# Optimization experiments

Measured on AMD Instinct MI355X. Metric: run time of the kernel, lower is better.

## Reference

```python
import jax, jax.numpy as jnp
import numpy as np

B, L, IDIM = 2, 4096, 2048
N_HEADS, N_GROUPS, HEAD_DIM = 16, 4, 128
GROUP_SIZE = N_HEADS // N_GROUPS
WINDOW = 1024
SCALE = 256.0 ** -0.5  # query_pre_attn_scalar = 256
EPS = 1e-6


def setup_inputs() -> dict:
    key = jax.random.key(0)
    ks = jax.random.split(key, 8)
    x = jax.random.normal(ks[0], (B, L, IDIM), dtype=jnp.float32)
    # realistic RoPE tables
    inv_freq = 1.0 / (10000.0 ** (np.arange(0, HEAD_DIM, 2, dtype=np.float32) / HEAD_DIM))
    t = np.arange(L, dtype=np.float32)
    freqs = np.outer(t, inv_freq)                      # [L, HEAD_DIM//2]
    emb = np.concatenate([freqs, freqs], axis=-1)      # [L, HEAD_DIM]
    cos = jnp.asarray(np.cos(emb), dtype=jnp.float32)
    sin = jnp.asarray(np.sin(emb), dtype=jnp.float32)
    s = 0.02
    Wq = jax.random.normal(ks[1], (IDIM, N_HEADS * HEAD_DIM), dtype=jnp.float32) * s
    Wk = jax.random.normal(ks[2], (IDIM, N_GROUPS * HEAD_DIM), dtype=jnp.float32) * s
    Wv = jax.random.normal(ks[3], (IDIM, N_GROUPS * HEAD_DIM), dtype=jnp.float32) * s
    Wo = jax.random.normal(ks[4], (N_HEADS * HEAD_DIM, IDIM), dtype=jnp.float32) * s
    qn_w = jnp.ones((HEAD_DIM,), dtype=jnp.float32)
    kn_w = jnp.ones((HEAD_DIM,), dtype=jnp.float32)
    return {"x": x, "cos": cos, "sin": sin, "Wq": Wq, "Wk": Wk, "Wv": Wv, "Wo": Wo, "qn_w": qn_w, "kn_w": kn_w}


def _rmsnorm(x, w):
    var = jnp.mean(jnp.square(x), axis=-1, keepdims=True)
    return x * jax.lax.rsqrt(var + EPS) * w


def _rope(x, cos, sin):
    # x: [b, h, l, d]; cos/sin: [l, d]
    d2 = x.shape[-1] // 2
    x1, x2 = x[..., :d2], x[..., d2:]
    rot = jnp.concatenate([-x2, x1], axis=-1)
    return x * cos[None, None] + rot * sin[None, None]


def reference(x, cos, sin, Wq, Wk, Wv, Wo, qn_w, kn_w):
    b, l, _ = x.shape
    q = (x @ Wq).reshape(b, l, N_HEADS, HEAD_DIM).transpose(0, 2, 1, 3)   # b h l d
    k = (x @ Wk).reshape(b, l, N_GROUPS, HEAD_DIM).transpose(0, 2, 1, 3)  # b g l d
    v = (x @ Wv).reshape(b, l, N_GROUPS, HEAD_DIM).transpose(0, 2, 1, 3)  # b g l d
    q = _rmsnorm(q, qn_w)
    k = _rmsnorm(k, kn_w)
    q = _rope(q, cos, sin)
    k = _rope(k, cos, sin)
    k = jnp.repeat(k, GROUP_SIZE, axis=1)  # b h l d
    v = jnp.repeat(v, GROUP_SIZE, axis=1)
    dots = jnp.einsum('bhid,bhjd->bhij', q, k) * SCALE
    i = jnp.arange(l)[:, None]
    j = jnp.arange(l)[None, :]
    allowed = (j <= i) & (j > i - WINDOW)  # causal sliding window
    dots = jnp.where(allowed[None, None], dots, -jnp.inf)
    attn = jax.nn.softmax(dots, axis=-1)
    out = jnp.einsum('bhij,bhjd->bhid', attn, v)
    out = out.transpose(0, 2, 1, 3).reshape(b, l, N_HEADS * HEAD_DIM)
    return out @ Wo
```

## Files before the change

### kernel.cpp

```cpp
#include <hip/hip_runtime.h>
#include <hip/hip_bf16.h>

typedef __hip_bfloat16 bf16;
typedef __attribute__((ext_vector_type(8))) __bf16 bf16x8;
typedef __attribute__((ext_vector_type(4))) float f32x4;

#define MFMA16(a, b, c) __builtin_amdgcn_mfma_f32_16x16x32_bf16((a), (b), (c), 0, 0, 0)

static __device__ __forceinline__ void gload_lds16(const void* g, void* l) {
    typedef const __attribute__((address_space(1))) unsigned gq_t;
    typedef __attribute__((address_space(3))) unsigned ls_t;
    __builtin_amdgcn_global_load_lds((gq_t*)g, (ls_t*)l, 16, 0, 0);
}

__global__ __launch_bounds__(256) void cvt_bf16_kernel(const float* __restrict__ in,
                                                       bf16* __restrict__ out, int n) {
    int i = (blockIdx.x * 256 + threadIdx.x) * 8;
    if (i < n) {
        float4 a = *reinterpret_cast<const float4*>(in + i);
        float4 b = *reinterpret_cast<const float4*>(in + i + 4);
        bf16 tmp[8];
        tmp[0] = __float2bfloat16(a.x); tmp[1] = __float2bfloat16(a.y);
        tmp[2] = __float2bfloat16(a.z); tmp[3] = __float2bfloat16(a.w);
        tmp[4] = __float2bfloat16(b.x); tmp[5] = __float2bfloat16(b.y);
        tmp[6] = __float2bfloat16(b.z); tmp[7] = __float2bfloat16(b.w);
        *reinterpret_cast<uint4*>(out + i) = *reinterpret_cast<const uint4*>(tmp);
    }
}

__global__ __launch_bounds__(256) void transpose_wqkv_kernel(const float* __restrict__ Wq,
                                                             const float* __restrict__ Wk,
                                                             const float* __restrict__ Wv,
                                                             bf16* __restrict__ out) {
    __shared__ float tile[32][33];
    int k0 = blockIdx.x * 32;
    int n0 = blockIdx.y * 32;
    int tx = threadIdx.x & 31, ty = threadIdx.x >> 5;
#pragma unroll
    for (int i = 0; i < 4; ++i) {
        int k = k0 + ty + i * 8, n = n0 + tx;
        float v;
        if (n < 2048)      v = Wq[(size_t)k * 2048 + n];
        else if (n < 2560) v = Wk[(size_t)k * 512 + (n - 2048)];
        else               v = Wv[(size_t)k * 512 + (n - 2560)];
        tile[ty + i * 8][tx] = v;
    }
    __syncthreads();
#pragma unroll
    for (int i = 0; i < 4; ++i)
        out[(size_t)(n0 + ty + i * 8) * 2048 + k0 + tx] = __float2bfloat16(tile[tx][ty + i * 8]);
}

__global__ __launch_bounds__(256) void transpose_w_kernel(const float* __restrict__ in,
                                                          bf16* __restrict__ out) {
    __shared__ float tile[32][33];
    int k0 = blockIdx.x * 32, n0 = blockIdx.y * 32;
    int tx = threadIdx.x & 31, ty = threadIdx.x >> 5;
#pragma unroll
    for (int i = 0; i < 4; ++i)
        tile[ty + i * 8][tx] = in[(size_t)(k0 + ty + i * 8) * 2048 + n0 + tx];
    __syncthreads();
#pragma unroll
    for (int i = 0; i < 4; ++i)
        out[(size_t)(n0 + ty + i * 8) * 2048 + k0 + tx] = __float2bfloat16(tile[tx][ty + i * 8]);
}

template <int NFRAG, bool OUT_F32>
__global__ __launch_bounds__(512, 2) void gemm8p_kernel(const bf16* __restrict__ A,
                                                        const bf16* __restrict__ BT,
                                                        void* __restrict__ Cv,
                                                        int M, int N, int K, int nbn) {
    constexpr int BN = NFRAG * 64;
    constexpr int PB = NFRAG;
    __shared__ bf16 As[2][256 * 64];
    __shared__ bf16 Bs[2][BN * 64];
    int t = threadIdx.x;
    int lane = t & 63, w = t >> 6;
    int wm = w >> 2, wn = w & 3;
    int lr = lane & 15, lq = lane >> 4;
    int lin = blockIdx.x;
    int cpx = gridDim.x >> 3;
    int wg = (lin & 7) * cpx + (lin >> 3);
    int bm = wg / nbn, bn = wg % nbn;
    const bf16* Ab = A + (size_t)bm * 256 * K;
    const bf16* Bb = BT + (size_t)bn * BN * K;

    auto stA = [&](int slot, int kt, int piece) {
        int idx = piece * 512 + t;
        int r = idx >> 3, c8 = idx & 7;
        gload_lds16(Ab + (size_t)r * K + kt * 64 + ((c8 ^ (r & 7)) * 8), &As[slot][idx * 8]);
    };
    auto stB = [&](int slot, int kt, int piece) {
        int idx = piece * 512 + t;
        int r = idx >> 3, c8 = idx & 7;
        gload_lds16(Bb + (size_t)r * K + kt * 64 + ((c8 ^ (r & 7)) * 8), &Bs[slot][idx * 8]);
    };

    f32x4 acc[8][NFRAG] = {};
    bf16x8 bq[NFRAG][2], af[2][2];

    auto readB = [&](int slot) {
#pragma unroll
        for (int n = 0; n < NFRAG; ++n)
#pragma unroll
            for (int ks = 0; ks < 2; ++ks) {
                int ro = wn * (NFRAG * 16) + n * 16 + lr;
                int ch = (ks * 4 + lq) ^ (ro & 7);
                bq[n][ks] = *reinterpret_cast<const bf16x8*>(&Bs[slot][ro * 64 + ch * 8]);
            }
    };
    auto readA = [&](int mbase, int slot) {
#pragma unroll
        for (int mi = 0; mi < 2; ++mi)
#pragma unroll
            for (int ks = 0; ks < 2; ++ks) {
                int ro = wm * 128 + (mbase + mi) * 16 + lr;
                int ch = (ks * 4 + lq) ^ (ro & 7);
                af[mi][ks] = *reinterpret_cast<const bf16x8*>(&As[slot][ro * 64 + ch * 8]);
            }
    };
    auto mf = [&](int mbase) {
#pragma unroll
        for (int mi = 0; mi < 2; ++mi)
#pragma unroll
            for (int n = 0; n < NFRAG; ++n)
#pragma unroll
                for (int ks = 0; ks < 2; ++ks)
                    acc[mbase + mi][n] = MFMA16(af[mi][ks], bq[n][ks], acc[mbase + mi][n]);
    };

#define GATE_PB()                                                          \
    do {                                                                   \
        if constexpr (NFRAG == 4) asm volatile("s_waitcnt vmcnt(4)" ::: "memory"); \
        else                      asm volatile("s_waitcnt vmcnt(3)" ::: "memory"); \
    } while (0)
#define PHASE_TAIL()                                                       \
    do {                                                                   \
        __builtin_amdgcn_s_barrier();                                      \
        asm volatile("s_waitcnt lgkmcnt(0)" ::: "memory");                 \
    } while (0)
#define MFMA_CLUSTER(mb)                                                   \
    do {                                                                   \
        __builtin_amdgcn_s_setprio(1);                                     \
        mf(mb);                                                            \
        __builtin_amdgcn_s_setprio(0);                                     \
        __builtin_amdgcn_s_barrier();                                      \
    } while (0)

    int nkt = K >> 6;
#pragma unroll
    for (int p = 0; p < 4; ++p) stA(0, 0, p);
#pragma unroll
    for (int p = 0; p < PB; ++p) stB(0, 0, p);
#pragma unroll
    for (int p = 0; p < PB; ++p) stB(1, 1, p);
    GATE_PB();
    __builtin_amdgcn_s_barrier();

    int nI = nkt >> 1;
    for (int I = 0; I < nI; ++I) {
        int T = I << 1;
        bool s2 = (T + 2) < nkt, s3 = (T + 3) < nkt;
        readB(0); readA(0, 0);
#pragma unroll
        for (int p = 0; p < 4; ++p) stA(1, T + 1, p);
        PHASE_TAIL();
        MFMA_CLUSTER(0);
        readA(2, 0);
        if (s2) { stB(0, T + 2, 0); stB(0, T + 2, 1); }
        PHASE_TAIL();
        MFMA_CLUSTER(2);
        readA(4, 0);
        if (s2) {
#pragma unroll
            for (int p = 2; p < PB; ++p) stB(0, T + 2, p);
        }
        PHASE_TAIL();
        MFMA_CLUSTER(4);
        readA(6, 0);
        if (s2) GATE_PB();
        else    asm volatile("s_waitcnt vmcnt(0)" ::: "memory");
        PHASE_TAIL();
        MFMA_CLUSTER(6);
        readB(1); readA(0, 1);
        if (s2) {
#pragma unroll
            for (int p = 0; p < 4; ++p) stA(0, T + 2, p);
        }
        PHASE_TAIL();
        MFMA_CLUSTER(0);
        readA(2, 1);
        if (s3) { stB(1, T + 3, 0); stB(1, T + 3, 1); }
        PHASE_TAIL();
        MFMA_CLUSTER(2);
        readA(4, 1);
        if (s3) {
#pragma unroll
            for (int p = 2; p < PB; ++p) stB(1, T + 3, p);
        }
        PHASE_TAIL();
        MFMA_CLUSTER(4);
        readA(6, 1);
        if (s3) GATE_PB();
        else    asm volatile("s_waitcnt vmcnt(0)" ::: "memory");
        PHASE_TAIL();
        MFMA_CLUSTER(6);
    }
#undef GATE_PB
#undef PHASE_TAIL
#undef MFMA_CLUSTER

#pragma unroll
    for (int m = 0; m < 8; ++m)
#pragma unroll
        for (int n = 0; n < NFRAG; ++n) {
            int row = bm * 256 + wm * 128 + m * 16 + lq * 4;
            int col = bn * BN + wn * (NFRAG * 16) + n * 16 + lr;
#pragma unroll
            for (int j = 0; j < 4; ++j) {
                if (OUT_F32)
                    ((float*)Cv)[(size_t)(row + j) * N + col] = acc[m][n][j];
                else
                    ((bf16*)Cv)[(size_t)(row + j) * N + col] = __float2bfloat16(acc[m][n][j]);
            }
        }
}

__global__ __launch_bounds__(256) void normrope_kernel(const bf16* __restrict__ qkv,
                                                       const float* __restrict__ cosT,
                                                       const float* __restrict__ sinT,
                                                       const float* __restrict__ qnw,
                                                       const float* __restrict__ knw,
                                                       bf16* __restrict__ qh,
                                                       bf16* __restrict__ kh,
                                                       bf16* __restrict__ vt) {
    int t = threadIdx.x;
    int lane = t & 63, wv = t >> 6;
    int blk = blockIdx.x;
    int r = blk / 6;
    int s = (blk % 6) * 4 + wv;
    int b = r >> 12, l = r & 4095;
    const bf16* src = qkv + (size_t)r * 3072 + s * 128;
    float x1 = __bfloat162float(src[lane]);
    float x2 = __bfloat162float(src[lane + 64]);
    if (s < 20) {
        float ss = x1 * x1 + x2 * x2;
#pragma unroll
        for (int d = 1; d < 64; d <<= 1) ss += __shfl_xor(ss, d, 64);
        float rn = rsqrtf(ss * (1.0f / 128.0f) + 1e-6f);
        const float* wn = (s < 16) ? qnw : knw;
        float xn1 = x1 * rn * wn[lane];
        float xn2 = x2 * rn * wn[lane + 64];
        float c = cosT[(size_t)l * 128 + lane];
        float sn = sinT[(size_t)l * 128 + lane];
        float o1 = xn1 * c - xn2 * sn;
        float o2 = xn2 * c + xn1 * sn;
        if (s < 16) {
            const float scl = 0.0625f * 1.44269504088896f;
            bf16* dst = qh + ((size_t)(b * 16 + s) * 4096 + l) * 128;
            dst[lane] = __float2bfloat16(o1 * scl);
            dst[lane + 64] = __float2bfloat16(o2 * scl);
        } else {
            int g = s - 16;
            int sw = (l & 7) << 3;
            bf16* dst = kh + ((size_t)(b * 4 + g) * 4096 + l) * 128;
            dst[lane ^ sw] = __float2bfloat16(o1);
            dst[(lane + 64) ^ sw] = __float2bfloat16(o2);
        }
    } else {
        int g = s - 20;
        bf16* dst = vt + (size_t)(b * 4 + g) * 128 * 4096;
        int base = l & ~63, cj = l & 63;
        int d1 = lane, d2 = lane + 64;
        int sw = (lane & 7) << 3;
        dst[(size_t)d1 * 4096 + base + (cj ^ sw)] = __float2bfloat16(x1);
        dst[(size_t)d2 * 4096 + base + (cj ^ sw)] = __float2bfloat16(x2);
    }
}

__global__ __launch_bounds__(512, 4) void attn_kernel(const bf16* __restrict__ qh,
                                                      const bf16* __restrict__ kh,
                                                      const bf16* __restrict__ vt,
                                                      bf16* __restrict__ ao) {
    __shared__ bf16 Ks[2][64 * 128];
    __shared__ bf16 Vs[2][128 * 64];
    __shared__ bf16 P_lds[8][16][64];
    int t = threadIdx.x;
    int lane = t & 63, w = t >> 6;
    int lr = lane & 15, lq = lane >> 4;
    int qs = blockIdx.x * 128;
    int bh = blockIdx.y;
    int b = bh >> 4, h = bh & 15, g = h >> 2;
    const bf16* qp = qh + ((size_t)(b * 16 + h) * 4096 + qs + w * 16) * 128;
    const bf16* kp = kh + (size_t)(b * 4 + g) * 4096 * 128;
    const bf16* vp = vt + (size_t)(b * 4 + g) * 128 * 4096;

    bf16x8 aq[4];
#pragma unroll
    for (int kk = 0; kk < 4; ++kk)
        aq[kk] = *reinterpret_cast<const bf16x8*>(qp + (size_t)lr * 128 + kk * 32 + lq * 8);

    f32x4 o[8] = {};
    float lsum[4] = {0.f, 0.f, 0.f, 0.f};
    int row0 = qs + w * 16;
    int iq0 = row0 + lq * 4;
    int t0w = max(0, row0 - 1023) >> 6;
    int t1w = row0 >> 6;
    int t0 = max(0, qs - 1023) >> 6;
    int t1 = (qs + 112) >> 6;

    auto stage = [&](int buf, int kt) {
        int j0 = kt * 64;
        const bf16* kg = kp + (size_t)j0 * 128;
#pragma unroll
        for (int i = 0; i < 2; ++i) {
            int c = i * 512 + t;
            gload_lds16(kg + c * 8, &Ks[buf][c * 8]);
        }
#pragma unroll
        for (int i = 0; i < 2; ++i) {
            int c = i * 512 + t;
            int d = c >> 3, co = (c & 7) * 8;
            gload_lds16(vp + (size_t)d * 4096 + j0 + co, &Vs[buf][c * 8]);
        }
    };

    stage(0, t0);
    __syncthreads();
    int cur = 0;

    for (int kt = t0; kt <= t1; ++kt) {
        int j0 = kt * 64;
        if (kt < t1) stage(cur ^ 1, kt + 1);
        if (kt >= t0w && kt <= t1w) {
            f32x4 s[4] = {};
            __builtin_amdgcn_s_setprio(1);
#pragma unroll
            for (int jt = 0; jt < 4; ++jt) {
                int r = jt * 16 + lr;
                int rs = (r & 7) << 3;
#pragma unroll
                for (int kk = 0; kk < 4; ++kk) {
                    int c = kk * 32 + lq * 8;
                    bf16x8 bk = *reinterpret_cast<const bf16x8*>(&Ks[cur][r * 128 + (c ^ rs)]);
                    s[jt] = MFMA16(aq[kk], bk, s[jt]);
                }
            }
            __builtin_amdgcn_s_setprio(0);
            if (kt <= t0w + 1 || kt == t1w) {
#pragma unroll
                for (int jt = 0; jt < 4; ++jt)
#pragma unroll
                    for (int j = 0; j < 4; ++j) {
                        int qi = iq0 + j;
                        int kj = j0 + jt * 16 + lr;
                        if (!(kj <= qi && kj > qi - 1024)) s[jt][j] = -1e30f;
                    }
            }
#pragma unroll
            for (int jt = 0; jt < 4; ++jt)
#pragma unroll
                for (int j = 0; j < 4; ++j) {
                    float p = exp2f(s[jt][j] - 11.5415603f);
                    lsum[j] += p;
                    int row = lq * 4 + j;
                    P_lds[w][row][(jt * 16 + lr) ^ ((row & 7) << 3)] = __float2bfloat16(p);
                }
            __builtin_amdgcn_s_setprio(1);
#pragma unroll
            for (int kk2 = 0; kk2 < 2; ++kk2) {
                bf16x8 pa = *reinterpret_cast<const bf16x8*>(
                    &P_lds[w][lr][(kk2 * 32 + lq * 8) ^ ((lr & 7) << 3)]);
#pragma unroll
                for (int dt = 0; dt < 8; ++dt) {
                    int r = dt * 16 + lr;
                    int c = kk2 * 32 + lq * 8;
                    bf16x8 bv = *reinterpret_cast<const bf16x8*>(&Vs[cur][r * 64 + (c ^ ((r & 7) << 3))]);
                    o[dt] = MFMA16(pa, bv, o[dt]);
                }
            }
            __builtin_amdgcn_s_setprio(0);
        }
        __syncthreads();
        cur ^= 1;
    }
    float linv[4];
#pragma unroll
    for (int j = 0; j < 4; ++j) {
        float l = lsum[j];
        l += __shfl_xor(l, 1, 64);
        l += __shfl_xor(l, 2, 64);
        l += __shfl_xor(l, 4, 64);
        l += __shfl_xor(l, 8, 64);
        linv[j] = 1.0f / l;
    }
#pragma unroll
    for (int dt = 0; dt < 8; ++dt)
#pragma unroll
        for (int j = 0; j < 4; ++j) {
            float val = o[dt][j] * linv[j];
            ao[((size_t)(b * 4096 + qs + w * 16 + lq * 4 + j)) * 2048 + h * 128 + dt * 16 + lr] =
                __float2bfloat16(val);
        }
}

extern "C" void kernel_launch(void* const* d_in, const int* in_sizes, int n_in,
                              void* d_out, int out_size, void* d_ws, size_t ws_size,
                              hipStream_t stream) {
    const float* x    = (const float*)d_in[0];
    const float* cosT = (const float*)d_in[1];
    const float* sinT = (const float*)d_in[2];
    const float* Wq   = (const float*)d_in[3];
    const float* Wk   = (const float*)d_in[4];
    const float* Wv   = (const float*)d_in[5];
    const float* Wo   = (const float*)d_in[6];
    const float* qnw  = (const float*)d_in[7];
    const float* knw  = (const float*)d_in[8];

    char* ws = (char*)d_ws;
    bf16* xb    = (bf16*)(ws);
    bf16* wqkvT = (bf16*)(ws + 33554432);
    bf16* woT   = (bf16*)(ws + 46137344);
    bf16* qh    = (bf16*)(ws + 54525952);
    bf16* kh    = (bf16*)(ws + 88080384);
    bf16* vt    = (bf16*)(ws + 96468992);
    bf16* ao    = xb;
    bf16* qkv   = (bf16*)d_out;

    cvt_bf16_kernel<<<8192, 256, 0, stream>>>(x, xb, 16777216);
    transpose_wqkv_kernel<<<dim3(64, 96), 256, 0, stream>>>(Wq, Wk, Wv, wqkvT);
    transpose_w_kernel<<<dim3(64, 64), 256, 0, stream>>>(Wo, woT);
    gemm8p_kernel<3, false><<<512, 512, 0, stream>>>(xb, wqkvT, (void*)qkv, 8192, 3072, 2048, 16);
    normrope_kernel<<<49152, 256, 0, stream>>>(qkv, cosT, sinT, qnw, knw, qh, kh, vt);
    attn_kernel<<<dim3(32, 32), 512, 0, stream>>>(qh, kh, vt, ao);
    gemm8p_kernel<4, true><<<256, 512, 0, stream>>>(ao, woT, d_out, 8192, 2048, 2048, 8);
}
```

Before: 361.9 us.

## Keep P in registers via transposed QK^T MFMA and permuted V layout

The attention kernel computes S^T by swapping the MFMA operands, so each lane holds a row's scores in the layout the PV MFMA's A operand needs. The probabilities are packed to bf16 in registers instead of going through a per-wave LDS buffer. The normrope kernel permutes the V-transposed key positions to match, and vectorises its loads and stores with a shuffle-based rotate. This removes LDS writes, reads and waits on the softmax path, but relies on the key permutation being consistent across both kernels.

```diff
diff --git a/kernel.cpp b/kernel.cpp
--- a/kernel.cpp
+++ b/kernel.cpp
@@ -11,6 +11,11 @@
     typedef const __attribute__((address_space(1))) unsigned gq_t;
     typedef __attribute__((address_space(3))) unsigned ls_t;
     __builtin_amdgcn_global_load_lds((gq_t*)g, (ls_t*)l, 16, 0, 0);
+}
+
+static __device__ __forceinline__ unsigned short f2bfbits(float f) {
+    bf16 h = __float2bfloat16(f);
+    return *reinterpret_cast<unsigned short*>(&h);
 }
 
 __global__ __launch_bounds__(256) void cvt_bf16_kernel(const float* __restrict__ in,
@@ -240,41 +245,51 @@
     int r = blk / 6;
     int s = (blk % 6) * 4 + wv;
     int b = r >> 12, l = r & 4095;
+    int e0 = lane * 2;
     const bf16* src = qkv + (size_t)r * 3072 + s * 128;
-    float x1 = __bfloat162float(src[lane]);
-    float x2 = __bfloat162float(src[lane + 64]);
+    ushort2 xu = *reinterpret_cast<const ushort2*>(src + e0);
+    float v0 = __uint_as_float((unsigned)xu.x << 16);
+    float v1 = __uint_as_float((unsigned)xu.y << 16);
     if (s < 20) {
-        float ss = x1 * x1 + x2 * x2;
+        float ss = v0 * v0 + v1 * v1;
 #pragma unroll
         for (int d = 1; d < 64; d <<= 1) ss += __shfl_xor(ss, d, 64);
         float rn = rsqrtf(ss * (1.0f / 128.0f) + 1e-6f);
         const float* wn = (s < 16) ? qnw : knw;
-        float xn1 = x1 * rn * wn[lane];
-        float xn2 = x2 * rn * wn[lane + 64];
-        float c = cosT[(size_t)l * 128 + lane];
-        float sn = sinT[(size_t)l * 128 + lane];
-        float o1 = xn1 * c - xn2 * sn;
-        float o2 = xn2 * c + xn1 * sn;
+        float2 wv2 = *reinterpret_cast<const float2*>(wn + e0);
+        float xn0 = v0 * rn * wv2.x;
+        float xn1 = v1 * rn * wv2.y;
+        float xp0 = __shfl_xor(xn0, 32, 64);
+        float xp1 = __shfl_xor(xn1, 32, 64);
+        float r0 = (lane < 32) ? -xp0 : xp0;
+        float r1 = (lane < 32) ? -xp1 : xp1;
+        float2 c2 = *reinterpret_cast<const float2*>(cosT + (size_t)l * 128 + e0);
+        float2 s2 = *reinterpret_cast<const float2*>(sinT + (size_t)l * 128 + e0);
+        float o0 = xn0 * c2.x + r0 * s2.x;
+        float o1 = xn1 * c2.y + r1 * s2.y;
+        ushort2 ou;
         if (s < 16) {
             const float scl = 0.0625f * 1.44269504088896f;
+            ou.x = f2bfbits(o0 * scl);
+            ou.y = f2bfbits(o1 * scl);
             bf16* dst = qh + ((size_t)(b * 16 + s) * 4096 + l) * 128;
-            dst[lane] = __float2bfloat16(o1 * scl);
-            dst[lane + 64] = __float2bfloat16(o2 * scl);
+            *reinterpret_cast<ushort2*>(dst + e0) = ou;
         } else {
             int g = s - 16;
+            ou.x = f2bfbits(o0);
+            ou.y = f2bfbits(o1);
             int sw = (l & 7) << 3;
             bf16* dst = kh + ((size_t)(b * 4 + g) * 4096 + l) * 128;
-            dst[lane ^ sw] = __float2bfloat16(o1);
-            dst[(lane + 64) ^ sw] = __float2bfloat16(o2);
+            *reinterpret_cast<ushort2*>(dst + (e0 ^ sw)) = ou;
         }
     } else {
         int g = s - 20;
         bf16* dst = vt + (size_t)(b * 4 + g) * 128 * 4096;
         int base = l & ~63, cj = l & 63;
-        int d1 = lane, d2 = lane + 64;
-        int sw = (lane & 7) << 3;
-        dst[(size_t)d1 * 4096 + base + (cj ^ sw)] = __float2bfloat16(x1);
-        dst[(size_t)d2 * 4096 + base + (cj ^ sw)] = __float2bfloat16(x2);
+        int pos = (cj & 0x23) | ((cj & 16) >> 2) | ((cj & 12) << 1);
+        int d0 = e0, d1 = e0 + 1;
+        dst[(size_t)d0 * 4096 + base + (pos ^ ((d0 & 7) << 3))] = __float2bfloat16(v0);
+        dst[(size_t)d1 * 4096 + base + (pos ^ ((d1 & 7) << 3))] = __float2bfloat16(v1);
     }
 }
 
@@ -284,7 +299,6 @@
                                                       bf16* __restrict__ ao) {
     __shared__ bf16 Ks[2][64 * 128];
     __shared__ bf16 Vs[2][128 * 64];
-    __shared__ bf16 P_lds[8][16][64];
     int t = threadIdx.x;
     int lane = t & 63, w = t >> 6;
     int lr = lane & 15, lq = lane >> 4;
@@ -301,9 +315,9 @@
         aq[kk] = *reinterpret_cast<const bf16x8*>(qp + (size_t)lr * 128 + kk * 32 + lq * 8);
 
     f32x4 o[8] = {};
-    float lsum[4] = {0.f, 0.f, 0.f, 0.f};
+    float lsum = 0.f;
     int row0 = qs + w * 16;
-    int iq0 = row0 + lq * 4;
+    int qi = row0 + lr;
     int t0w = max(0, row0 - 1023) >> 6;
     int t1w = row0 >> 6;
     int t0 = max(0, qs - 1023) >> 6;
@@ -343,7 +357,7 @@
                 for (int kk = 0; kk < 4; ++kk) {
                     int c = kk * 32 + lq * 8;
                     bf16x8 bk = *reinterpret_cast<const bf16x8*>(&Ks[cur][r * 128 + (c ^ rs)]);
-                    s[jt] = MFMA16(aq[kk], bk, s[jt]);
+                    s[jt] = MFMA16(bk, aq[kk], s[jt]);
                 }
             }
             __builtin_amdgcn_s_setprio(0);
@@ -352,31 +366,34 @@
                 for (int jt = 0; jt < 4; ++jt)
 #pragma unroll
                     for (int j = 0; j < 4; ++j) {
-                        int qi = iq0 + j;
-                        int kj = j0 + jt * 16 + lr;
+                        int kj = j0 + jt * 16 + lq * 4 + j;
                         if (!(kj <= qi && kj > qi - 1024)) s[jt][j] = -1e30f;
                     }
             }
+            unsigned pk[4][2];
 #pragma unroll
             for (int jt = 0; jt < 4; ++jt)
 #pragma unroll
-                for (int j = 0; j < 4; ++j) {
-                    float p = exp2f(s[jt][j] - 11.5415603f);
-                    lsum[j] += p;
-                    int row = lq * 4 + j;
-                    P_lds[w][row][(jt * 16 + lr) ^ ((row & 7) << 3)] = __float2bfloat16(p);
+                for (int hh = 0; hh < 2; ++hh) {
+                    float p0 = exp2f(s[jt][2 * hh] - 11.5415603f);
+                    float p1 = exp2f(s[jt][2 * hh + 1] - 11.5415603f);
+                    lsum += p0 + p1;
+                    asm("v_cvt_pk_bf16_f32 %0, %1, %2" : "=v"(pk[jt][hh]) : "v"(p0), "v"(p1));
                 }
             __builtin_amdgcn_s_setprio(1);
 #pragma unroll
             for (int kk2 = 0; kk2 < 2; ++kk2) {
-                bf16x8 pa = *reinterpret_cast<const bf16x8*>(
-                    &P_lds[w][lr][(kk2 * 32 + lq * 8) ^ ((lr & 7) << 3)]);
+                union { unsigned u[4]; bf16x8 v; } pu;
+                pu.u[0] = pk[2 * kk2][0];
+                pu.u[1] = pk[2 * kk2][1];
+                pu.u[2] = pk[2 * kk2 + 1][0];
+                pu.u[3] = pk[2 * kk2 + 1][1];
 #pragma unroll
                 for (int dt = 0; dt < 8; ++dt) {
                     int r = dt * 16 + lr;
                     int c = kk2 * 32 + lq * 8;
                     bf16x8 bv = *reinterpret_cast<const bf16x8*>(&Vs[cur][r * 64 + (c ^ ((r & 7) << 3))]);
-                    o[dt] = MFMA16(pa, bv, o[dt]);
+                    o[dt] = MFMA16(pu.v, bv, o[dt]);
                 }
             }
             __builtin_amdgcn_s_setprio(0);
@@ -384,22 +401,20 @@
         __syncthreads();
         cur ^= 1;
     }
-    float linv[4];
-#pragma unroll
-    for (int j = 0; j < 4; ++j) {
-        float l = lsum[j];
-        l += __shfl_xor(l, 1, 64);
-        l += __shfl_xor(l, 2, 64);
-        l += __shfl_xor(l, 4, 64);
-        l += __shfl_xor(l, 8, 64);
-        linv[j] = 1.0f / l;
-    }
+    float lt = lsum;
+    lt += __shfl_xor(lt, 16, 64);
+    lt += __shfl_xor(lt, 32, 64);
+    float linv = 1.0f / lt;
+    float lv[4];
+#pragma unroll
+    for (int j = 0; j < 4; ++j)
+        lv[j] = __shfl(linv, lq * 4 + j, 64);
 #pragma unroll
     for (int dt = 0; dt < 8; ++dt)
 #pragma unroll
         for (int j = 0; j < 4; ++j) {
-            float val = o[dt][j] * linv[j];
-            ao[((size_t)(b * 4096 + qs + w * 16 + lq * 4 + j)) * 2048 + h * 128 + dt * 16 + lr] =
+            float val = o[dt][j] * lv[j];
+            ao[((size_t)(b * 4096 + row0 + lq * 4 + j)) * 2048 + h * 128 + dt * 16 + lr] =
                 __float2bfloat16(val);
         }
 }
```

Result: no change. 357.0 us (-1.4%).
